# Performance work log

Hardware: AMD Instinct MI355X
Metric: run time of the kernel (lower is better)

Reference implementation:

```python
import jax, jax.numpy as jnp
import numpy as np
import math

HID = 300   # model dim (d_k in the source's scale factor)
HDIM = 64   # attention projection dim
NH = 8      # heads = last axis of view(B,S,HDIM//8,8)
DH = HDIM // NH
L = 6


def pos_encoding(S, d):
    pos = jnp.arange(S, dtype=jnp.float32)[:, None]
    i = jnp.arange(d)
    expo = jnp.where(i % 2 == 0, i, i - 1).astype(jnp.float32) / d
    ang = pos / jnp.power(jnp.float32(10000.0), expo)  # (S, d)
    return jnp.where(i % 2 == 0, jnp.sin(ang), jnp.cos(ang))


def norm(x, g, b):
    mu = jnp.mean(x, axis=-1, keepdims=True)
    var = jnp.var(x, axis=-1, keepdims=True, ddof=1)  # torch.var is unbiased
    return g * (x - mu) / jnp.sqrt(var + 1e-8) + b


def mha(x, mask, wq, wk, wv, wo):
    B, S, _ = x.shape
    # view(B,S,DH,NH).permute(3,0,1,2): head h = feature indices i*NH+h
    q = (x @ wq).reshape(B, S, DH, NH).transpose(3, 0, 1, 2)  # (NH,B,S,DH)
    k = (x @ wk).reshape(B, S, DH, NH).transpose(3, 0, 1, 2)
    v = (x @ wv).reshape(B, S, DH, NH).transpose(3, 0, 1, 2)
    e = jnp.einsum('hbqd,hbkd->hbqk', q, k) / math.sqrt(HID)
    e = jnp.where(mask[None], jnp.float32(-1e9), e)
    alpha = jax.nn.softmax(e, axis=-1)
    h = jnp.einsum('hbqk,hbkd->hbqd', alpha, v)
    # cat(head0..head7, dim=2) -> head-major feature layout
    a = h.transpose(1, 2, 0, 3).reshape(B, S, HDIM)
    return a @ wo


def encoder(x, mask, wq, wk, wv, wo, w1, bb1, w2, bb2, g1, be1, g2, be2):
    x2 = mha(x, mask, wq, wk, wv, wo)
    x = norm(x2 + x, g1, be1)
    ff = jnp.maximum(x @ w1 + bb1, 0.0) @ w2 + bb2
    x = norm(ff + x, g2, be2)
    return x


def setup_inputs() -> dict:
    key = jax.random.key(0)
    ks = jax.random.split(key, 16)
    B, S, V, C = 32, 512, 50000, 1000
    sc = 0.02
    return {
        'x': jax.random.randint(ks[0], (B, S), 0, V),
        'emb': jax.random.normal(ks[1], (V, HID), jnp.float32) * sc,
        'WQ': jax.random.normal(ks[2], (L, HID, HDIM), jnp.float32) * sc,
        'WK': jax.random.normal(ks[3], (L, HID, HDIM), jnp.float32) * sc,
        'WV': jax.random.normal(ks[4], (L, HID, HDIM), jnp.float32) * sc,
        'WO': jax.random.normal(ks[5], (L, HDIM, HID), jnp.float32) * sc,
        'W1': jax.random.normal(ks[6], (L, HID, 4 * HID), jnp.float32) * sc,
        'b1': jax.random.normal(ks[7], (L, 4 * HID), jnp.float32) * sc,
        'W2': jax.random.normal(ks[8], (L, 4 * HID, HID), jnp.float32) * sc,
        'b2': jax.random.normal(ks[9], (L, HID), jnp.float32) * sc,
        'gamma1': jnp.ones((L,), jnp.float32),
        'beta1': jnp.zeros((L,), jnp.float32),
        'gamma2': jnp.ones((L,), jnp.float32),
        'beta2': jnp.zeros((L,), jnp.float32),
        'V_d': jax.random.normal(ks[10], (HID, C), jnp.float32) * sc,
        'gamma_f': jnp.float32(1.0),
        'beta_f': jnp.float32(0.0),
    }


def reference(x, emb, WQ, WK, WV, WO, W1, b1, W2, b2,
              gamma1, beta1, gamma2, beta2, V_d, gamma_f, beta_f):
    B, S = x.shape
    mask = (x == 0)[:, None, :] * jnp.ones((1, S, 1), bool)  # (B,S,S)
    x1 = emb[x]                               # (B,S,HID)
    x2 = x1 + pos_encoding(S, HID)[None]
    acc = x2 + x1                             # dense residual running sum
    out = x2
    for l in range(L):
        out = encoder(acc, mask, WQ[l], WK[l], WV[l], WO[l],
                      W1[l], b1[l], W2[l], b2[l],
                      gamma1[l], beta1[l], gamma2[l], beta2[l])
        acc = acc + out
    logits = jnp.sum(out, axis=1) @ V_d       # (B,C)
    return jax.nn.softmax(norm(logits, gamma_f, beta_f), axis=1)
```

## Files before the change

### kernel.cpp

```cpp
#include <hip/hip_runtime.h>
#include <hip/hip_bf16.h>
#include <cstdio>
#include <cstdint>

#define BATCH 32
#define SEQ 512
#define BSQ (BATCH*SEQ)
#define HIDD 300
#define HD 64
#define NHEAD 8
#define DHEAD 8
#define NLAYERS 6
#define FFD 1200
#define NCLS 1000
#define NSPLIT 4
#define KCH (SEQ/NSPLIT)
#define QKVP 256
#define CLS_KS 4
#define CLS_KC (HIDD/CLS_KS)

typedef short short8 __attribute__((ext_vector_type(8)));
typedef float floatx4 __attribute__((ext_vector_type(4)));

__device__ __forceinline__ short f2b(float v){
  __hip_bfloat16 h = __float2bfloat16(v);
  short s; __builtin_memcpy(&s, &h, 2); return s;
}
__device__ __forceinline__ unsigned pk2(float a, float b){
  return (unsigned)(unsigned short)f2b(a) | ((unsigned)(unsigned short)f2b(b) << 16);
}

__global__ void t10_embed(const int* __restrict__ toks,
                          const float* __restrict__ emb,
                          float* __restrict__ acc,
                          short* __restrict__ accbf){
  int idx = blockIdx.x*256 + threadIdx.x;
  if (idx >= BSQ*320) return;
  int row = idx / 320;
  int j   = idx - row*320;
  if (j >= HIDD){ accbf[(size_t)row*320 + j] = 0; return; }
  int t = toks[row];
  float e = emb[(size_t)t*HIDD + j];
  int s = row & (SEQ-1);
  float expo = (float)(j & ~1) * (1.0f/(float)HIDD);
  float ang  = (float)s * expf(-expo * 9.210340371976184f);
  float pe   = (j & 1) ? cosf(ang) : sinf(ang);
  float v = 2.0f*e + pe;
  acc[(size_t)row*HIDD + j] = v;
  accbf[(size_t)row*320 + j] = f2b(v);
}

__global__ void prep_w(const float* __restrict__ src, short* __restrict__ dst,
                       int K, int N, int Kpad, int rows, int nbase,
                       int sls, int dls, int total, int perm, float smul){
  int idx = blockIdx.x*256 + threadIdx.x;
  if (idx >= total) return;
  int l   = idx / (rows*Kpad);
  int rem = idx - l*(rows*Kpad);
  int n = rem / Kpad;
  int k = rem - n*Kpad;
  int sc = perm ? ((n & 7)*8 + (n >> 3)) : n;
  float v = (n < N && k < K) ? src[(size_t)l*sls + (size_t)k*N + sc]*smul : 0.f;
  dst[(size_t)l*dls + (size_t)(nbase+n)*Kpad + k] = f2b(v);
}

__global__ __launch_bounds__(256) void mm_a16(
    const short* __restrict__ A, const short* __restrict__ Wt,
    const float* __restrict__ bias, float* __restrict__ C,
    short* __restrict__ Cb,
    int M, int N, int Kpad, int Npad, int nnb, int relu){
  __shared__ short sA[64][40];
  __shared__ short sB[64][40];
  int wg = blockIdx.x;
  int cpx = gridDim.x >> 3;
  int swz = (wg & 7)*cpx + (wg >> 3);
  int mt = swz / nnb, nt = swz - mt*nnb;
  int m0 = mt*64, n0 = nt*64;
  int tid = threadIdx.x;
  int lane = tid & 63, wv = tid >> 6;
  int wm = (wv & 1)*32, wn = (wv >> 1)*32;
  int l15 = lane & 15, quad = lane >> 4;
  floatx4 acc[2][2] = {};
  int srow = tid >> 2, sko = (tid & 3)*8;
  const short* Arow = A  + (size_t)(m0 + srow)*Kpad + sko;
  const short* Brow = Wt + (size_t)(n0 + srow)*Kpad + sko;
  int nch = Kpad >> 5;
  for (int c = 0; c < nch; c++){
    int k0 = c*32;
    __syncthreads();
    *(short8*)&sA[srow][sko] = *(const short8*)(Arow + k0);
    *(short8*)&sB[srow][sko] = *(const short8*)(Brow + k0);
    __syncthreads();
    short8 af[2], bf[2];
    for (int i=0;i<2;i++)
      af[i] = *(const short8*)&sA[wm + i*16 + l15][quad*8];
    for (int j=0;j<2;j++)
      bf[j] = *(const short8*)&sB[wn + j*16 + l15][quad*8];
    for (int i=0;i<2;i++)
      for (int j=0;j<2;j++)
        acc[i][j] = __builtin_amdgcn_mfma_f32_16x16x32_bf16(af[i], bf[j], acc[i][j], 0,0,0);
  }
  if (Cb){
    for (int j=0;j<2;j++){
      int n = n0 + wn + j*16 + l15;
      float bv = (bias && n < N) ? bias[n] : 0.f;
      for (int i=0;i<2;i++){
        int mbase = m0 + wm + i*16 + quad*4;
        for (int r=0;r<4;r++){
          float cv = acc[i][j][r] + bv;
          if (relu) cv = fmaxf(cv, 0.f);
          Cb[(size_t)(mbase+r)*Npad + n] = (n < N) ? f2b(cv) : (short)0;
        }
      }
    }
  } else {
    for (int j=0;j<2;j++){
      int n = n0 + wn + j*16 + l15;
      if (n >= N) continue;
      float bv = bias ? bias[n] : 0.f;
      for (int i=0;i<2;i++){
        int mbase = m0 + wm + i*16 + quad*4;
        for (int r=0;r<4;r++){
          float cv = acc[i][j][r] + bv;
          if (relu) cv = fmaxf(cv, 0.f);
          C[(size_t)(mbase+r)*N + n] = cv;
        }
      }
    }
  }
}

__global__ __launch_bounds__(256) void mm64(
    const short* __restrict__ A, const short* __restrict__ Wt,
    const float* __restrict__ bias, float* __restrict__ C,
    short* __restrict__ Cb,
    int M, int N, int Kpad, int Npad, int nnb, int relu){
  __shared__ short sA[64][40];
  __shared__ short sB[128][40];
  int wg = blockIdx.x;
  int cpx = gridDim.x >> 3;
  int swz = (wg & 7)*cpx + (wg >> 3);
  int mt = swz / nnb, nt = swz - mt*nnb;
  int m0 = mt*64, n0 = nt*128;
  int tid = threadIdx.x;
  int lane = tid & 63, wv = tid >> 6;
  int l15 = lane & 15, quad = lane >> 4;
  int wn = wv*32;
  floatx4 acc[4][2] = {};
  int lr = tid >> 2, lc = (tid & 3)*8;
  const short* Arow  = A  + (size_t)(m0 + lr)*Kpad + lc;
  const short* Brow0 = Wt + (size_t)(n0 + lr)*Kpad + lc;
  const short* Brow1 = Wt + (size_t)(n0 + 64 + lr)*Kpad + lc;
  int nch = Kpad >> 5;
  for (int c = 0; c < nch; c++){
    int k0 = c*32;
    short8 va  = *(const short8*)(Arow  + k0);
    short8 vb0 = *(const short8*)(Brow0 + k0);
    short8 vb1 = *(const short8*)(Brow1 + k0);
    __syncthreads();
    *(short8*)&sA[lr][lc]      = va;
    *(short8*)&sB[lr][lc]      = vb0;
    *(short8*)&sB[64+lr][lc]   = vb1;
    __syncthreads();
    short8 af[4], bf[2];
    #pragma unroll
    for (int i=0;i<4;i++)
      af[i] = *(const short8*)&sA[i*16 + l15][quad*8];
    #pragma unroll
    for (int j=0;j<2;j++)
      bf[j] = *(const short8*)&sB[wn + j*16 + l15][quad*8];
    #pragma unroll
    for (int i=0;i<4;i++)
      #pragma unroll
      for (int j=0;j<2;j++)
        acc[i][j] = __builtin_amdgcn_mfma_f32_16x16x32_bf16(af[i], bf[j], acc[i][j], 0,0,0);
  }
  if (Cb){
    #pragma unroll
    for (int j=0;j<2;j++){
      int n = n0 + wn + j*16 + l15;
      float bv = (bias && n < N) ? bias[n] : 0.f;
      #pragma unroll
      for (int i=0;i<4;i++){
        int mbase = m0 + i*16 + quad*4;
        #pragma unroll
        for (int r=0;r<4;r++){
          float cv = acc[i][j][r] + bv;
          if (relu) cv = fmaxf(cv, 0.f);
          Cb[(size_t)(mbase+r)*Npad + n] = (n < N) ? f2b(cv) : (short)0;
        }
      }
    }
  } else {
    #pragma unroll
    for (int j=0;j<2;j++){
      int n = n0 + wn + j*16 + l15;
      if (n >= N) continue;
      float bv = bias ? bias[n] : 0.f;
      #pragma unroll
      for (int i=0;i<4;i++){
        int mbase = m0 + i*16 + quad*4;
        #pragma unroll
        for (int r=0;r<4;r++){
          float cv = acc[i][j][r] + bv;
          if (relu) cv = fmaxf(cv, 0.f);
          C[(size_t)(mbase+r)*N + n] = cv;
        }
      }
    }
  }
}

__global__ __launch_bounds__(256) void mm64k(
    const short* __restrict__ A, const short* __restrict__ Wt,
    const float* __restrict__ bias, float* __restrict__ C0,
    float* __restrict__ C1,
    int M, int N, int ldK, int klen, int nnb){
  __shared__ short sA[64][40];
  __shared__ short sB[128][40];
  int wg = blockIdx.x;
  int cpx = gridDim.x >> 3;
  int swz = (wg & 7)*cpx + (wg >> 3);
  int ksl = swz & 1;
  int t2  = swz >> 1;
  int mt = t2 / nnb, nt = t2 - mt*nnb;
  int m0 = mt*64, n0 = nt*128;
  int koff = ksl*klen;
  int tid = threadIdx.x;
  int lane = tid & 63, wv = tid >> 6;
  int l15 = lane & 15, quad = lane >> 4;
  int wn = wv*32;
  floatx4 acc[4][2] = {};
  int lr = tid >> 2, lc = (tid & 3)*8;
  const short* Arow  = A  + (size_t)(m0 + lr)*ldK + koff + lc;
  const short* Brow0 = Wt + (size_t)(n0 + lr)*ldK + koff + lc;
  const short* Brow1 = Wt + (size_t)(n0 + 64 + lr)*ldK + koff + lc;
  int nch = klen >> 5;
  for (int c = 0; c < nch; c++){
    int k0 = c*32;
    short8 va  = *(const short8*)(Arow  + k0);
    short8 vb0 = *(const short8*)(Brow0 + k0);
    short8 vb1 = *(const short8*)(Brow1 + k0);
    __syncthreads();
    *(short8*)&sA[lr][lc]      = va;
    *(short8*)&sB[lr][lc]      = vb0;
    *(short8*)&sB[64+lr][lc]   = vb1;
    __syncthreads();
    short8 af[4], bf[2];
    #pragma unroll
    for (int i=0;i<4;i++)
      af[i] = *(const short8*)&sA[i*16 + l15][quad*8];
    #pragma unroll
    for (int j=0;j<2;j++)
      bf[j] = *(const short8*)&sB[wn + j*16 + l15][quad*8];
    #pragma unroll
    for (int i=0;i<4;i++)
      #pragma unroll
      for (int j=0;j<2;j++)
        acc[i][j] = __builtin_amdgcn_mfma_f32_16x16x32_bf16(af[i], bf[j], acc[i][j], 0,0,0);
  }
  float* C = ksl ? C1 : C0;
  const float* bs = ksl ? nullptr : bias;
  #pragma unroll
  for (int j=0;j<2;j++){
    int n = n0 + wn + j*16 + l15;
    if (n >= N) continue;
    float bv = bs ? bs[n] : 0.f;
    #pragma unroll
    for (int i=0;i<4;i++){
      int mbase = m0 + i*16 + quad*4;
      #pragma unroll
      for (int r=0;r<4;r++)
        C[(size_t)(mbase+r)*N + n] = acc[i][j][r] + bv;
    }
  }
}

__global__ __launch_bounds__(256) void mm128p(
    const short* __restrict__ A, const short* __restrict__ Wt,
    const float* __restrict__ bias, float* __restrict__ C,
    short* __restrict__ Cb,
    int M, int N, int Kpad, int Npad, int nnb, int relu){
  __shared__ short sA[128][40];
  __shared__ short sB[128][40];
  int wg = blockIdx.x;
  int cpx = gridDim.x >> 3;
  int swz = (wg & 7)*cpx + (wg >> 3);
  int mt = swz / nnb, nt = swz - mt*nnb;
  int m0 = mt*128, n0 = nt*128;
  int tid = threadIdx.x;
  int lane = tid & 63, wv = tid >> 6;
  int wm = (wv & 1)*64, wn = (wv >> 1)*64;
  int l15 = lane & 15, quad = lane >> 4;
  floatx4 acc[4][4] = {};
  int lr = tid >> 2, lc = (tid & 3)*8;
  const short* Arow0 = A  + (size_t)(m0 + lr)*Kpad + lc;
  const short* Arow1 = A  + (size_t)(m0 + 64 + lr)*Kpad + lc;
  const short* Brow0 = Wt + (size_t)(n0 + lr)*Kpad + lc;
  const short* Brow1 = Wt + (size_t)(n0 + 64 + lr)*Kpad + lc;
  int nch = Kpad >> 5;
  for (int c = 0; c < nch; c++){
    int k0 = c*32;
    short8 va0 = *(const short8*)(Arow0 + k0);
    short8 va1 = *(const short8*)(Arow1 + k0);
    short8 vb0 = *(const short8*)(Brow0 + k0);
    short8 vb1 = *(const short8*)(Brow1 + k0);
    __syncthreads();
    *(short8*)&sA[lr][lc]    = va0;
    *(short8*)&sA[64+lr][lc] = va1;
    *(short8*)&sB[lr][lc]    = vb0;
    *(short8*)&sB[64+lr][lc] = vb1;
    __syncthreads();
    short8 af[4], bf[4];
    #pragma unroll
    for (int i=0;i<4;i++)
      af[i] = *(const short8*)&sA[wm + i*16 + l15][quad*8];
    #pragma unroll
    for (int j=0;j<4;j++)
      bf[j] = *(const short8*)&sB[wn + j*16 + l15][quad*8];
    #pragma unroll
    for (int i=0;i<4;i++)
      #pragma unroll
      for (int j=0;j<4;j++)
        acc[i][j] = __builtin_amdgcn_mfma_f32_16x16x32_bf16(af[i], bf[j], acc[i][j], 0,0,0);
  }
  if (Cb){
    #pragma unroll
    for (int j=0;j<4;j++){
      int n = n0 + wn + j*16 + l15;
      float bv = (bias && n < N) ? bias[n] : 0.f;
      #pragma unroll
      for (int i=0;i<4;i++){
        int mbase = m0 + wm + i*16 + quad*4;
        #pragma unroll
        for (int r=0;r<4;r++){
          float cv = acc[i][j][r] + bv;
          if (relu) cv = fmaxf(cv, 0.f);
          Cb[(size_t)(mbase+r)*Npad + n] = (n < N) ? f2b(cv) : (short)0;
        }
      }
    }
  } else {
    #pragma unroll
    for (int j=0;j<4;j++){
      int n = n0 + wn + j*16 + l15;
      if (n >= N) continue;
      float bv = bias ? bias[n] : 0.f;
      #pragma unroll
      for (int i=0;i<4;i++){
        int mbase = m0 + wm + i*16 + quad*4;
        #pragma unroll
        for (int r=0;r<4;r++){
          float cv = acc[i][j][r] + bv;
          if (relu) cv = fmaxf(cv, 0.f);
          C[(size_t)(mbase+r)*N + n] = cv;
        }
      }
    }
  }
}

__global__ __launch_bounds__(256) void t18_attn(
    const short* __restrict__ qkvb, const int* __restrict__ toks,
    float* __restrict__ pp, float* __restrict__ ps){
  __shared__ short vb16[KCH][16];
  __shared__ float msk[KCH];
  __shared__ short Pl[4][16][136];
  int blk = blockIdx.x;
  int ks = blk & (NSPLIT-1);
  int bh = blk >> 2;
  int b = bh >> 3, h = bh & 7;
  int tid = threadIdx.x;
  int lane = tid & 63, w = tid >> 6;
  int quad = lane >> 4, l15 = lane & 15;
  int kbase = ks*KCH;
  if (tid < KCH){
    *(short8*)&vb16[tid][0] =
      *(const short8*)(qkvb + (size_t)(b*SEQ + kbase + tid)*QKVP + 128 + h*8);
  } else {
    int r = tid - KCH;
    msk[r] = (toks[b*SEQ + kbase + r]==0) ? -1e9f : 0.f;
  }
  __syncthreads();

  short8 kfrag[8];
  #pragma unroll
  for (int kt=0;kt<8;kt++){
    short8 f;
    #pragma unroll
    for (int j=0;j<8;j++) f[j] = 0;
    if (quad == 0)
      f = *(const short8*)(qkvb + (size_t)(b*SEQ + kbase + kt*16 + l15)*QKVP + 64 + h*8);
    kfrag[kt] = f;
  }
  short8 vfrag[4];
  #pragma unroll
  for (int ks2=0;ks2<4;ks2++){
    short8 f;
    #pragma unroll
    for (int j=0;j<8;j++) f[j] = 0;
    if (l15 < 8){
      #pragma unroll
      for (int j=0;j<8;j++) f[j] = vb16[ks2*32 + quad*8 + j][l15];
    } else if (l15 == 8){
      #pragma unroll
      for (int j=0;j<8;j++) f[j] = (short)0x3F80;
    }
    vfrag[ks2] = f;
  }

  for (int t = 0; t < 8; t++){
    int q0 = w*128 + t*16;
    short8 qf;
    #pragma unroll
    for (int j=0;j<8;j++) qf[j] = 0;
    if (quad == 0)
      qf = *(const short8*)(qkvb + (size_t)(b*SEQ + q0 + l15)*QKVP + h*8);
    #pragma unroll
    for (int kt2 = 0; kt2 < 4; kt2++){
      floatx4 z = {0.f,0.f,0.f,0.f};
      floatx4 a0 = __builtin_amdgcn_mfma_f32_16x16x32_bf16(kfrag[2*kt2],   qf, z, 0,0,0);
      floatx4 a1 = __builtin_amdgcn_mfma_f32_16x16x32_bf16(kfrag[2*kt2+1], qf, z, 0,0,0);
      float p0[4], p1[4];
      #pragma unroll
      for (int r=0;r<4;r++){
        float m0 = msk[(2*kt2)*16   + quad*4 + r];
        float m1 = msk[(2*kt2+1)*16 + quad*4 + r];
        p0[r] = __expf(fminf(a0[r] + m0, 60.f));
        p1[r] = __expf(fminf(a1[r] + m1, 60.f));
      }
      uint2 u0, u1;
      u0.x = pk2(p0[0], p0[1]); u0.y = pk2(p0[2], p0[3]);
      u1.x = pk2(p1[0], p1[1]); u1.y = pk2(p1[2], p1[3]);
      *(uint2*)&Pl[w][l15][(2*kt2)*16   + quad*4] = u0;
      *(uint2*)&Pl[w][l15][(2*kt2+1)*16 + quad*4] = u1;
    }
    floatx4 o = {0.f,0.f,0.f,0.f};
    #pragma unroll
    for (int ks2=0; ks2<4; ks2++){
      short8 pa = *(const short8*)&Pl[w][l15][ks2*32 + quad*8];
      o = __builtin_amdgcn_mfma_f32_16x16x32_bf16(pa, vfrag[ks2], o, 0,0,0);
    }
    if (l15 < 8){
      #pragma unroll
      for (int r=0;r<4;r++){
        int q = q0 + quad*4 + r;
        pp[(size_t)ks*BSQ*64 + (size_t)(b*SEQ+q)*64 + h*8 + l15] = o[r];
      }
    } else if (l15 == 8){
      #pragma unroll
      for (int r=0;r<4;r++){
        int q = q0 + quad*4 + r;
        ps[(size_t)ks*BSQ*8 + (size_t)(b*SEQ+q)*8 + h] = o[r];
      }
    }
  }
}

__global__ __launch_bounds__(256) void t12_attn_comb(
    const float* __restrict__ pp, const float* __restrict__ ps,
    short* __restrict__ aout){
  int idx = blockIdx.x*256 + threadIdx.x;
  if (idx >= BSQ*8) return;
  float s = 0.f;
  for (int k=0;k<NSPLIT;k++) s += ps[(size_t)k*BSQ*8 + idx];
  float inv = 1.f/s;
  int bsq = idx >> 3, h = idx & 7;
  size_t base = (size_t)bsq*64 + h*8;
  float o[8] = {};
  for (int k=0;k<NSPLIT;k++){
    const float4* p = (const float4*)(pp + (size_t)k*BSQ*64 + base);
    float4 a = p[0], bq = p[1];
    o[0]+=a.x; o[1]+=a.y; o[2]+=a.z; o[3]+=a.w;
    o[4]+=bq.x; o[5]+=bq.y; o[6]+=bq.z; o[7]+=bq.w;
  }
  short8 r;
  for (int d=0;d<8;d++) r[d] = f2b(o[d]*inv);
  *(short8*)(aout + base) = r;
}

__global__ __launch_bounds__(256) void t18_addnorm(
                 const float* __restrict__ xa, const float* __restrict__ xb,
                 const float* __restrict__ xc,
                 float* __restrict__ y, short* __restrict__ ybf,
                 float* __restrict__ accum, short* __restrict__ accbf,
                 const float* __restrict__ gamma, const float* __restrict__ beta,
                 int l){
  int w = threadIdx.x >> 6, lane = threadIdx.x & 63;
  int row = blockIdx.x*4 + w;
  size_t base  = (size_t)row*HIDD;
  size_t bbase = (size_t)row*320;
  float v[5];
  float s = 0.f, sq = 0.f;
  #pragma unroll
  for (int t=0;t<5;t++){
    int j = lane + t*64;
    float x = 0.f;
    if (j < HIDD){
      x = xa[base+j];
      if (xb) x += xb[base+j];
      if (xc) x += xc[base+j];
    }
    v[t] = x; s += x; sq += x*x;
  }
  #pragma unroll
  for (int off=32; off; off>>=1){ s += __shfl_down(s,off); sq += __shfl_down(sq,off); }
  s = __shfl(s, 0); sq = __shfl(sq, 0);
  float mu  = s * (1.0f/HIDD);
  float var = (sq - (float)HIDD*mu*mu) * (1.0f/(HIDD-1));
  float rstd = rsqrtf(var + 1e-8f);
  float g = gamma[l], be = beta[l];
  #pragma unroll
  for (int t=0;t<5;t++){
    int j = lane + t*64;
    if (j < HIDD){
      float o = g*(v[t]-mu)*rstd + be;
      if (y) y[base+j] = o;
      if (ybf) ybf[bbase+j] = f2b(o);
      if (accum){
        float a = accum[base+j] + o;
        accum[base+j] = a;
        if (accbf) accbf[bbase+j] = f2b(a);
      }
    } else if (j < 320){
      if (ybf) ybf[bbase+j] = 0;
      if (accbf) accbf[bbase+j] = 0;
    }
  }
}

__global__ __launch_bounds__(256) void t13_colsum_part(
    const float* __restrict__ outb, float* __restrict__ part){
  int blk = blockIdx.x;
  int b = blk >> 3, c = blk & 7;
  int tid = threadIdx.x;
  size_t base = (size_t)b*SEQ*HIDD + (size_t)c*64*HIDD;
  int j1 = tid + 256;
  float s0 = 0.f, s1 = 0.f;
  for (int t = 0; t < 64; t++){
    const float* row = outb + base + (size_t)t*HIDD;
    s0 += row[tid];
    if (j1 < HIDD) s1 += row[j1];
  }
  float* dst = part + (size_t)(c*BATCH + b)*HIDD;
  dst[tid] = s0;
  if (j1 < HIDD) dst[j1] = s1;
}

__global__ void t13_colsum_comb(const float* __restrict__ part,
                                float* __restrict__ sums){
  int idx = blockIdx.x*256 + threadIdx.x;
  if (idx >= BATCH*HIDD) return;
  float s = 0.f;
  for (int c = 0; c < 8; c++) s += part[(size_t)c*BATCH*HIDD + idx];
  sums[idx] = s;
}

__global__ __launch_bounds__(256) void t13_cls(
    const float* __restrict__ sums, const float* __restrict__ W,
    float* __restrict__ plog){
  int gid = blockIdx.x*256 + threadIdx.x;
  if (gid >= CLS_KS*BATCH*NCLS) return;
  int c = gid / (BATCH*NCLS);
  int rem = gid - c*(BATCH*NCLS);
  int m = rem / NCLS, n = rem - m*NCLS;
  const float* arow = sums + m*HIDD + c*CLS_KC;
  const float* wcol = W + (size_t)c*CLS_KC*NCLS + n;
  float acc = 0.f;
  #pragma unroll 5
  for (int k = 0; k < CLS_KC; k++)
    acc = fmaf(arow[k], wcol[(size_t)k*NCLS], acc);
  plog[gid] = acc;
}

__device__ __forceinline__ float t10_bsum(float val, float* red){
  for (int off=32; off; off>>=1) val += __shfl_down(val, off);
  __syncthreads();
  if ((threadIdx.x & 63)==0) red[threadIdx.x>>6] = val;
  __syncthreads();
  return red[0]+red[1]+red[2]+red[3];
}
__device__ __forceinline__ float t10_bmax(float val, float* red){
  for (int off=32; off; off>>=1) val = fmaxf(val, __shfl_down(val, off));
  __syncthreads();
  if ((threadIdx.x & 63)==0) red[threadIdx.x>>6] = val;
  __syncthreads();
  return fmaxf(fmaxf(red[0],red[1]), fmaxf(red[2],red[3]));
}

__global__ __launch_bounds__(256) void t10_final(
                  const float* __restrict__ plog,
                  const float* __restrict__ gf, const float* __restrict__ bff,
                  float* __restrict__ outp){
  __shared__ float red[4];
  int b = blockIdx.x, tid = threadIdx.x;
  size_t base = (size_t)b*NCLS;
  float v[4];
  float s = 0.f, sq = 0.f;
  for (int t=0;t<4;t++){
    int j = tid + t*256;
    float x = 0.f;
    if (j < NCLS){
      for (int c=0;c<CLS_KS;c++) x += plog[(size_t)c*BATCH*NCLS + base + j];
    }
    v[t] = x; s += x; sq += x*x;
  }
  s  = t10_bsum(s, red);
  sq = t10_bsum(sq, red);
  float mu  = s * (1.0f/NCLS);
  float var = (sq - (float)NCLS*mu*mu) * (1.0f/(NCLS-1));
  float rstd = rsqrtf(var + 1e-8f);
  float g = gf[0], be = bff[0];
  float y[4]; float mx = -1e30f;
  for (int t=0;t<4;t++){
    int j = tid + t*256;
    y[t] = g*(v[t]-mu)*rstd + be;
    if (j < NCLS) mx = fmaxf(mx, y[t]);
  }
  mx = t10_bmax(mx, red);
  float p[4]; float es = 0.f;
  for (int t=0;t<4;t++){
    int j = tid + t*256;
    p[t] = (j < NCLS) ? __expf(y[t]-mx) : 0.f;
    es += p[t];
  }
  es = t10_bsum(es, red);
  float inv = 1.0f/es;
  for (int t=0;t<4;t++){
    int j = tid + t*256;
    if (j < NCLS) outp[base+j] = p[t]*inv;
  }
}

extern "C" void kernel_launch(void* const* d_in, const int* in_sizes, int n_in,
                              void* d_out, int out_size, void* d_ws, size_t ws_size,
                              hipStream_t stream){
  const int*   toks = (const int*)d_in[0];
  const float* emb  = (const float*)d_in[1];
  const float* WQ   = (const float*)d_in[2];
  const float* WK   = (const float*)d_in[3];
  const float* WV   = (const float*)d_in[4];
  const float* WO   = (const float*)d_in[5];
  const float* W1   = (const float*)d_in[6];
  const float* b1   = (const float*)d_in[7];
  const float* W2   = (const float*)d_in[8];
  const float* b2   = (const float*)d_in[9];
  const float* g1   = (const float*)d_in[10];
  const float* be1  = (const float*)d_in[11];
  const float* g2   = (const float*)d_in[12];
  const float* be2  = (const float*)d_in[13];
  const float* Vd   = (const float*)d_in[14];
  const float* gf   = (const float*)d_in[15];
  const float* bff  = (const float*)d_in[16];
  float* outp = (float*)d_out;

  float* acc    = (float*)d_ws;
  float* xn     = acc    + (size_t)BSQ*HIDD;
  float* outb   = xn     + (size_t)BSQ*HIDD;
  float* tmp    = outb   + (size_t)BSQ*HIDD;
  float* qkv    = tmp    + (size_t)BSQ*HIDD;
  float* sums   = qkv    + (size_t)BSQ*192;
  float* logits = sums   + BATCH*HIDD;
  short* qkv_bf = (short*)qkv;
  float* pp     = tmp;
  float* ps     = tmp + (size_t)NSPLIT*BSQ*64;
  short* acc_bf = (short*)(logits + BATCH*NCLS);
  short* xn_bf  = acc_bf + (size_t)BSQ*320;
  short* aat_bf = xn_bf  + (size_t)BSQ*320;
  short* ff1_bf = aat_bf + (size_t)BSQ*64;
  short* wqkv = ff1_bf + (size_t)BSQ*1280;
  short* wo   = wqkv + (size_t)6*256*320;
  short* w1t  = wo   + (size_t)6*384*64;
  short* w2t  = w1t  + (size_t)6*1280*320;
  float* cspart = (float*)(w2t + (size_t)6*384*1280);
  float* plog   = cspart + (size_t)8*BATCH*HIDD;

  {
    const float kscale = 0.057735026918962574f;
    int tq = 6*64*320;
    prep_w<<<(tq+255)/256,256,0,stream>>>(WQ, wqkv, 300, 64, 320, 64, 0,   19200, 81920, tq, 1, 1.0f);
    prep_w<<<(tq+255)/256,256,0,stream>>>(WK, wqkv, 300, 64, 320, 64, 64,  19200, 81920, tq, 1, kscale);
    prep_w<<<(tq+255)/256,256,0,stream>>>(WV, wqkv, 300, 64, 320, 64, 128, 19200, 81920, tq, 1, 1.0f);
    prep_w<<<(tq+255)/256,256,0,stream>>>(WQ, wqkv, 300, 0,  320, 64, 192, 19200, 81920, tq, 0, 1.0f);
    int to = 6*384*64;
    prep_w<<<(to+255)/256,256,0,stream>>>(WO, wo, 64, 300, 64, 384, 0, 19200, 24576, to, 0, 1.0f);
    int t1 = 6*1280*320;
    prep_w<<<(t1+255)/256,256,0,stream>>>(W1, w1t, 300, 1200, 320, 1280, 0, 360000, 409600, t1, 0, 1.0f);
    int t2 = 6*384*1280;
    prep_w<<<(t2+255)/256,256,0,stream>>>(W2, w2t, 1200, 300, 1280, 384, 0, 360000, 491520, t2, 0, 1.0f);
  }

  t10_embed<<<(BSQ*320+255)/256, 256, 0, stream>>>(toks, emb, acc, acc_bf);

  for (int l = 0; l < NLAYERS; l++){
    mm64<<<256*2,256,0,stream>>>(acc_bf, wqkv + (size_t)l*81920, nullptr, nullptr, qkv_bf,
                                 BSQ, 192, 320, QKVP, 2, 0);
    t18_attn<<<BATCH*NHEAD*NSPLIT, 256, 0, stream>>>(qkv_bf, toks, pp, ps);
    t12_attn_comb<<<(BSQ*8)/256, 256, 0, stream>>>(pp, ps, aat_bf);
    mm_a16<<<256*5,256,0,stream>>>(aat_bf, wo + (size_t)l*24576, nullptr, tmp, nullptr,
                                   BSQ, 300, 64, 0, 5, 0);
    t18_addnorm<<<BSQ/4,256,0,stream>>>(tmp, acc, nullptr, xn, xn_bf, nullptr, nullptr, g1, be1, l);
    mm128p<<<128*10,256,0,stream>>>(xn_bf, w1t + (size_t)l*409600, b1 + (size_t)l*FFD,
                                    nullptr, ff1_bf, BSQ, 1200, 320, 1280, 10, 1);
    mm64k<<<2*256*3,256,0,stream>>>(ff1_bf, w2t + (size_t)l*491520, b2 + (size_t)l*HIDD,
                                    tmp, outb, BSQ, 300, 1280, 640, 3);
    t18_addnorm<<<BSQ/4,256,0,stream>>>(tmp, xn, outb, (l==NLAYERS-1)?outb:nullptr, nullptr,
                                        (l==NLAYERS-1)?nullptr:acc,
                                        (l==NLAYERS-1)?nullptr:acc_bf, g2, be2, l);
  }

  t13_colsum_part<<<BATCH*8, 256, 0, stream>>>(outb, cspart);
  t13_colsum_comb<<<(BATCH*HIDD+255)/256, 256, 0, stream>>>(cspart, sums);
  t13_cls<<<(CLS_KS*BATCH*NCLS)/256, 256, 0, stream>>>(sums, Vd, plog);
  t10_final<<<BATCH, 256, 0, stream>>>(plog, gf, bff, outp);

  hipStreamCaptureStatus cs = hipStreamCaptureStatusNone;
  hipStreamIsCapturing(stream, &cs);
  if (cs == hipStreamCaptureStatusNone){
    hipError_t e_sync = hipStreamSynchronize(stream);
    float ho[4] = {-1,-1,-1,-1};
    hipMemcpy(ho, d_out, 16, hipMemcpyDeviceToHost);
    fprintf(stderr, "[t20] sync=%s out[0..3]=%g,%g,%g,%g\n",
            hipGetErrorString(e_sync), ho[0], ho[1], ho[2], ho[3]);
    fflush(stderr);
  }
}
```

Before: 1.107 ms.

## Drop split-K in FF2 GEMM and use 64-wide K chunks

Replaces the split-K FF2 GEMM, which wrote two partial outputs that the following add-norm then summed, with a single full-K kernel. Each block now stages 64-wide K chunks in shared memory, halving the number of barrier pairs per tile. The second partial buffer write and read disappear, but grid size drops from 1536 to 768 blocks and each block runs twice as long, so occupancy and latency hiding may suffer. The larger LDS tiles also reduce how many blocks fit per CU.

```diff
diff --git a/kernel.cpp b/kernel.cpp
--- a/kernel.cpp
+++ b/kernel.cpp
@@ -211,61 +211,65 @@
   }
 }
 
-__global__ __launch_bounds__(256) void mm64k(
+__global__ __launch_bounds__(256) void mm64b(
     const short* __restrict__ A, const short* __restrict__ Wt,
-    const float* __restrict__ bias, float* __restrict__ C0,
-    float* __restrict__ C1,
-    int M, int N, int ldK, int klen, int nnb){
-  __shared__ short sA[64][40];
-  __shared__ short sB[128][40];
+    const float* __restrict__ bias, float* __restrict__ C,
+    int M, int N, int Kpad, int nnb){
+  __shared__ short sA[64][72];
+  __shared__ short sB[128][72];
   int wg = blockIdx.x;
   int cpx = gridDim.x >> 3;
   int swz = (wg & 7)*cpx + (wg >> 3);
-  int ksl = swz & 1;
-  int t2  = swz >> 1;
-  int mt = t2 / nnb, nt = t2 - mt*nnb;
+  int mt = swz / nnb, nt = swz - mt*nnb;
   int m0 = mt*64, n0 = nt*128;
-  int koff = ksl*klen;
   int tid = threadIdx.x;
   int lane = tid & 63, wv = tid >> 6;
   int l15 = lane & 15, quad = lane >> 4;
   int wn = wv*32;
   floatx4 acc[4][2] = {};
-  int lr = tid >> 2, lc = (tid & 3)*8;
-  const short* Arow  = A  + (size_t)(m0 + lr)*ldK + koff + lc;
-  const short* Brow0 = Wt + (size_t)(n0 + lr)*ldK + koff + lc;
-  const short* Brow1 = Wt + (size_t)(n0 + 64 + lr)*ldK + koff + lc;
-  int nch = klen >> 5;
+  int lr = tid >> 2, lc = (tid & 3)*16;
+  const short* Arow  = A  + (size_t)(m0 + lr)*Kpad + lc;
+  const short* Brow0 = Wt + (size_t)(n0 + lr)*Kpad + lc;
+  const short* Brow1 = Wt + (size_t)(n0 + 64 + lr)*Kpad + lc;
+  int nch = Kpad >> 6;
   for (int c = 0; c < nch; c++){
-    int k0 = c*32;
-    short8 va  = *(const short8*)(Arow  + k0);
+    int k0 = c*64;
+    short8 va0 = *(const short8*)(Arow  + k0);
+    short8 va1 = *(const short8*)(Arow  + k0 + 8);
     short8 vb0 = *(const short8*)(Brow0 + k0);
-    short8 vb1 = *(const short8*)(Brow1 + k0);
+    short8 vb1 = *(const short8*)(Brow0 + k0 + 8);
+    short8 vc0 = *(const short8*)(Brow1 + k0);
+    short8 vc1 = *(const short8*)(Brow1 + k0 + 8);
     __syncthreads();
-    *(short8*)&sA[lr][lc]      = va;
-    *(short8*)&sB[lr][lc]      = vb0;
-    *(short8*)&sB[64+lr][lc]   = vb1;
+    *(short8*)&sA[lr][lc]       = va0;
+    *(short8*)&sA[lr][lc+8]     = va1;
+    *(short8*)&sB[lr][lc]       = vb0;
+    *(short8*)&sB[lr][lc+8]     = vb1;
+    *(short8*)&sB[64+lr][lc]    = vc0;
+    *(short8*)&sB[64+lr][lc+8]  = vc1;
     __syncthreads();
-    short8 af[4], bf[2];
-    #pragma unroll
-    for (int i=0;i<4;i++)
-      af[i] = *(const short8*)&sA[i*16 + l15][quad*8];
-    #pragma unroll
-    for (int j=0;j<2;j++)
-      bf[j] = *(const short8*)&sB[wn + j*16 + l15][quad*8];
-    #pragma unroll
-    for (int i=0;i<4;i++)
+    #pragma unroll
+    for (int h = 0; h < 2; h++){
+      int ko = h*32 + quad*8;
+      short8 af[4], bf[2];
+      #pragma unroll
+      for (int i=0;i<4;i++)
+        af[i] = *(const short8*)&sA[i*16 + l15][ko];
       #pragma unroll
       for (int j=0;j<2;j++)
-        acc[i][j] = __builtin_amdgcn_mfma_f32_16x16x32_bf16(af[i], bf[j], acc[i][j], 0,0,0);
-  }
-  float* C = ksl ? C1 : C0;
-  const float* bs = ksl ? nullptr : bias;
+        bf[j] = *(const short8*)&sB[wn + j*16 + l15][ko];
+      #pragma unroll
+      for (int i=0;i<4;i++)
+        #pragma unroll
+        for (int j=0;j<2;j++)
+          acc[i][j] = __builtin_amdgcn_mfma_f32_16x16x32_bf16(af[i], bf[j], acc[i][j], 0,0,0);
+    }
+  }
   #pragma unroll
   for (int j=0;j<2;j++){
     int n = n0 + wn + j*16 + l15;
     if (n >= N) continue;
-    float bv = bs ? bs[n] : 0.f;
+    float bv = bias ? bias[n] : 0.f;
     #pragma unroll
     for (int i=0;i<4;i++){
       int mbase = m0 + i*16 + quad*4;
@@ -702,9 +706,9 @@
     t18_addnorm<<<BSQ/4,256,0,stream>>>(tmp, acc, nullptr, xn, xn_bf, nullptr, nullptr, g1, be1, l);
     mm128p<<<128*10,256,0,stream>>>(xn_bf, w1t + (size_t)l*409600, b1 + (size_t)l*FFD,
                                     nullptr, ff1_bf, BSQ, 1200, 320, 1280, 10, 1);
-    mm64k<<<2*256*3,256,0,stream>>>(ff1_bf, w2t + (size_t)l*491520, b2 + (size_t)l*HIDD,
-                                    tmp, outb, BSQ, 300, 1280, 640, 3);
-    t18_addnorm<<<BSQ/4,256,0,stream>>>(tmp, xn, outb, (l==NLAYERS-1)?outb:nullptr, nullptr,
+    mm64b<<<256*3,256,0,stream>>>(ff1_bf, w2t + (size_t)l*491520, b2 + (size_t)l*HIDD,
+                                  tmp, BSQ, 300, 1280, 3);
+    t18_addnorm<<<BSQ/4,256,0,stream>>>(tmp, xn, nullptr, (l==NLAYERS-1)?outb:nullptr, nullptr,
                                         (l==NLAYERS-1)?nullptr:acc,
                                         (l==NLAYERS-1)?nullptr:acc_bf, g2, be2, l);
   }
@@ -720,7 +724,7 @@
     hipError_t e_sync = hipStreamSynchronize(stream);
     float ho[4] = {-1,-1,-1,-1};
     hipMemcpy(ho, d_out, 16, hipMemcpyDeviceToHost);
-    fprintf(stderr, "[t20] sync=%s out[0..3]=%g,%g,%g,%g\n",
+    fprintf(stderr, "[t22] sync=%s out[0..3]=%g,%g,%g,%g\n",
             hipGetErrorString(e_sync), ho[0], ho[1], ho[2], ho[3]);
     fflush(stderr);
   }
```

Result: faster. 1.046 ms (-5.4%).
